# Optimization experiments

Hardware: AMD Instinct MI355X
Metric: run time of the kernel (lower is better)

The kernel has to match this reference:

```python
import jax, jax.numpy as jnp
import numpy as np

B, H, D, S = 8, 12, 64, 1024


def setup_inputs() -> dict:
    key = jax.random.key(0)
    kq, kk, kv, km = jax.random.split(key, 4)
    Q = jax.random.normal(kq, (B, H, D, S), dtype=jnp.float32)
    K = jax.random.normal(kk, (B, H, D, S), dtype=jnp.float32)
    V = jax.random.normal(kv, (B, H, D, S), dtype=jnp.float32)
    atten_masks = jax.random.randint(km, (B, S), 0, 2, dtype=jnp.int32)
    return {"Q": Q, "K": K, "V": V, "atten_masks": atten_masks}


def reference(Q, K, V, atten_masks):
    # Q,K,V: [B, H, D, S] (feature-major layout as in the torch module)
    d_k = Q.shape[2]
    # scores = K^T @ Q / sqrt(d_k) -> [B, H, S_k, S_q]
    scores = jnp.einsum('bhds,bhdt->bhst', K, Q) / jnp.sqrt(jnp.float32(d_k))
    # mask [B, S] applies along the LAST axis (query index) after the cat-broadcast
    mask = atten_masks[:, None, None, :]  # [B,1,1,S] broadcasts to [B,H,S,S]
    scores = jnp.where(mask == 0, jnp.float32(-1e9), scores)
    # softmax over last dim (faithful to dim=-1 in the original)
    attn = jax.nn.softmax(scores, axis=-1)  # [B, H, S_k, S_q]
    # context = V @ attn -> [B, H, D, S_q]
    context = jnp.einsum('bhds,bhst->bhdt', V, attn)
    # transpose(-1,-2) -> [B, H, S, D]; concat heads along feature dim -> [B, S, H*D]
    context = jnp.transpose(context, (0, 3, 1, 2)).reshape(context.shape[0], context.shape[3], -1)
    return (context, attn)
```

## Files before the change

kernel.cpp:

```cpp
#include <hip/hip_runtime.h>
#include <stdint.h>


typedef __attribute__((ext_vector_type(8))) short short8;
typedef __attribute__((ext_vector_type(4))) float floatx4;

#define DEVINL __device__ __forceinline__

DEVINL uint32_t f2u(float x) { union { float f; uint32_t u; } c; c.f = x; return c.u; }
DEVINL float u2f(uint32_t u) { union { uint32_t u; float f; } c; c.u = u; return c.f; }

DEVINL void split_bf16(float x, short &hi, short &lo) {
  uint32_t u = f2u(x);
  uint32_t r = u + 0x7FFFu + ((u >> 16) & 1u);
  hi = (short)(r >> 16);
  float hf = u2f(r & 0xFFFF0000u);
  float lf = x - hf;
  uint32_t v = f2u(lf);
  uint32_t r2 = v + 0x7FFFu + ((v >> 16) & 1u);
  lo = (short)(r2 >> 16);
}

__global__ void k0_qtranspose(const float* __restrict__ Q, unsigned short* __restrict__ QT) {
  const int bh = blockIdx.y;
  const int t0 = blockIdx.x * 64;
  const int tid = threadIdx.x;
  __shared__ float tile[64][65];
  {
    const int d = tid >> 2;
    const int ts = (tid & 3) * 16;
    const float* src = Q + ((size_t)bh * 64 + d) * 1024 + t0 + ts;
    #pragma unroll
    for (int i = 0; i < 4; ++i) {
      float4 v = reinterpret_cast<const float4*>(src)[i];
      tile[d][ts + 4 * i + 0] = v.x;
      tile[d][ts + 4 * i + 1] = v.y;
      tile[d][ts + 4 * i + 2] = v.z;
      tile[d][ts + 4 * i + 3] = v.w;
    }
  }
  __syncthreads();
  {
    const int t = tid >> 2;
    const int dseg = (tid & 3) * 16;
    uint32_t hw[8], lw[8];
    #pragma unroll
    for (int jj = 0; jj < 8; ++jj) {
      short h0, l0, h1, l1;
      split_bf16(tile[dseg + 2 * jj + 0][t], h0, l0);
      split_bf16(tile[dseg + 2 * jj + 1][t], h1, l1);
      hw[jj] = (uint32_t)(uint16_t)h0 | ((uint32_t)(uint16_t)h1 << 16);
      lw[jj] = (uint32_t)(uint16_t)l0 | ((uint32_t)(uint16_t)l1 << 16);
    }
    unsigned short* orow = QT + ((size_t)bh * 1024 + t0 + t) * 128;
    uint4* oh = reinterpret_cast<uint4*>(orow + dseg);
    oh[0] = make_uint4(hw[0], hw[1], hw[2], hw[3]);
    oh[1] = make_uint4(hw[4], hw[5], hw[6], hw[7]);
    uint4* ol = reinterpret_cast<uint4*>(orow + 64 + dseg);
    ol[0] = make_uint4(lw[0], lw[1], lw[2], lw[3]);
    ol[1] = make_uint4(lw[4], lw[5], lw[6], lw[7]);
  }
}

__global__ __launch_bounds__(256, 2)
void k1_scores_softmax(const float* __restrict__ Kt, const int* __restrict__ masks,
                       const unsigned short* __restrict__ QT, float* __restrict__ attn) {
  const int bh = blockIdx.y;
  const int b = bh / 12;
  const int sblk = blockIdx.x;
  const int tid = threadIdx.x;
  const int wave = tid >> 6, lane = tid & 63;
  const int ws = wave >> 1, wt = wave & 1;
  const int q = lane >> 4, l15 = lane & 15;

  short8 ahi[2], alo[2];
  {
    const int sA = sblk * 32 + ws * 16 + l15;
    const float* Kp = Kt + (size_t)bh * 65536 + sA;
    #pragma unroll
    for (int kk = 0; kk < 2; ++kk)
      #pragma unroll
      for (int j = 0; j < 8; ++j) {
        short h, l;
        split_bf16(Kp[(size_t)(kk * 32 + q * 8 + j) * 1024], h, l);
        ahi[kk][j] = h; alo[kk][j] = l;
      }
  }

  floatx4 acc[8][4];
  #pragma unroll
  for (int i = 0; i < 8; ++i)
    #pragma unroll
    for (int j = 0; j < 4; ++j) acc[i][j] = (floatx4){0.f, 0.f, 0.f, 0.f};

  const unsigned short* QTb = QT + (size_t)bh * 1024 * 128;
  #pragma unroll
  for (int tt = 0; tt < 8; ++tt) {
    #pragma unroll
    for (int nf = 0; nf < 4; ++nf) {
      const int t = tt * 128 + wt * 64 + nf * 16 + l15;
      const unsigned short* row = QTb + (size_t)t * 128 + q * 8;
      #pragma unroll
      for (int kk = 0; kk < 2; ++kk) {
        short8 bh16 = *reinterpret_cast<const short8*>(row + kk * 32);
        short8 bl16 = *reinterpret_cast<const short8*>(row + 64 + kk * 32);
        acc[tt][nf] = __builtin_amdgcn_mfma_f32_16x16x32_bf16(ahi[kk], bh16, acc[tt][nf], 0, 0, 0);
        acc[tt][nf] = __builtin_amdgcn_mfma_f32_16x16x32_bf16(alo[kk], bh16, acc[tt][nf], 0, 0, 0);
        acc[tt][nf] = __builtin_amdgcn_mfma_f32_16x16x32_bf16(ahi[kk], bl16, acc[tt][nf], 0, 0, 0);
      }
    }
  }

  const int* mrow = masks + b * 1024;
  float mx[4] = {-3.0e38f, -3.0e38f, -3.0e38f, -3.0e38f};
  #pragma unroll
  for (int tt = 0; tt < 8; ++tt)
    #pragma unroll
    for (int nf = 0; nf < 4; ++nf) {
      const int t = tt * 128 + wt * 64 + nf * 16 + l15;
      const bool mk = (mrow[t] != 0);
      #pragma unroll
      for (int r = 0; r < 4; ++r) {
        float v = mk ? acc[tt][nf][r] * 0.125f : -1.0e9f;
        acc[tt][nf][r] = v;
        mx[r] = fmaxf(mx[r], v);
      }
    }
  #pragma unroll
  for (int r = 0; r < 4; ++r)
    #pragma unroll
    for (int off = 1; off < 16; off <<= 1)
      mx[r] = fmaxf(mx[r], __shfl_xor(mx[r], off, 16));

  __shared__ float redmax[2][32];
  __shared__ float redsum[2][32];
  const int srow = ws * 16 + q * 4;
  if (l15 == 0) {
    #pragma unroll
    for (int r = 0; r < 4; ++r) redmax[wt][srow + r] = mx[r];
  }
  __syncthreads();
  float fm[4];
  #pragma unroll
  for (int r = 0; r < 4; ++r) fm[r] = fmaxf(redmax[0][srow + r], redmax[1][srow + r]);

  float sm[4] = {0.f, 0.f, 0.f, 0.f};
  #pragma unroll
  for (int tt = 0; tt < 8; ++tt)
    #pragma unroll
    for (int nf = 0; nf < 4; ++nf)
      #pragma unroll
      for (int r = 0; r < 4; ++r) {
        float e = __expf(acc[tt][nf][r] - fm[r]);
        acc[tt][nf][r] = e;
        sm[r] += e;
      }
  #pragma unroll
  for (int r = 0; r < 4; ++r)
    #pragma unroll
    for (int off = 1; off < 16; off <<= 1)
      sm[r] += __shfl_xor(sm[r], off, 16);
  if (l15 == 0) {
    #pragma unroll
    for (int r = 0; r < 4; ++r) redsum[wt][srow + r] = sm[r];
  }
  __syncthreads();
  float inv[4];
  #pragma unroll
  for (int r = 0; r < 4; ++r) inv[r] = 1.0f / (redsum[0][srow + r] + redsum[1][srow + r]);

  float* arow = attn + (size_t)bh * 1024 * 1024;
  #pragma unroll
  for (int tt = 0; tt < 8; ++tt)
    #pragma unroll
    for (int nf = 0; nf < 4; ++nf) {
      const int t = tt * 128 + wt * 64 + nf * 16 + l15;
      #pragma unroll
      for (int r = 0; r < 4; ++r) {
        const int s = sblk * 32 + srow + r;
        arow[(size_t)s * 1024 + t] = acc[tt][nf][r] * inv[r];
      }
    }
}

__global__ __launch_bounds__(256, 2)
void k2_pv(const float* __restrict__ V, const float* __restrict__ attn, float* __restrict__ ctx) {
  const int bh = blockIdx.y;
  const int b = bh / 12, h = bh % 12;
  const int tblk = blockIdx.x;
  const int tid = threadIdx.x;
  const int wave = tid >> 6, lane = tid & 63;
  const int q = lane >> 4, l15 = lane & 15;
  const int twave = tblk * 128 + wave * 32;

  floatx4 acc[4][2];
  #pragma unroll
  for (int i = 0; i < 4; ++i)
    #pragma unroll
    for (int j = 0; j < 2; ++j) acc[i][j] = (floatx4){0.f, 0.f, 0.f, 0.f};

  const float* Vb = V + (size_t)bh * 65536;
  const float* Ab = attn + (size_t)bh * 1048576;

  for (int s0 = 0; s0 < 1024; s0 += 32) {
    short8 vhi[4], vlo[4];
    #pragma unroll
    for (int mf = 0; mf < 4; ++mf) {
      const float* p = Vb + (size_t)(mf * 16 + l15) * 1024 + s0 + q * 8;
      #pragma unroll
      for (int j = 0; j < 8; ++j) {
        short hh, ll; split_bf16(p[j], hh, ll);
        vhi[mf][j] = hh; vlo[mf][j] = ll;
      }
    }
    short8 phi[2], plo[2];
    #pragma unroll
    for (int nf = 0; nf < 2; ++nf) {
      const int t = twave + nf * 16 + l15;
      const float* ap = Ab + (size_t)(s0 + q * 8) * 1024 + t;
      #pragma unroll
      for (int j = 0; j < 8; ++j) {
        short hh, ll; split_bf16(ap[(size_t)j * 1024], hh, ll);
        phi[nf][j] = hh; plo[nf][j] = ll;
      }
    }
    #pragma unroll
    for (int mf = 0; mf < 4; ++mf)
      #pragma unroll
      for (int nf = 0; nf < 2; ++nf) {
        acc[mf][nf] = __builtin_amdgcn_mfma_f32_16x16x32_bf16(vhi[mf], phi[nf], acc[mf][nf], 0, 0, 0);
        acc[mf][nf] = __builtin_amdgcn_mfma_f32_16x16x32_bf16(vlo[mf], phi[nf], acc[mf][nf], 0, 0, 0);
        acc[mf][nf] = __builtin_amdgcn_mfma_f32_16x16x32_bf16(vhi[mf], plo[nf], acc[mf][nf], 0, 0, 0);
      }
  }
  #pragma unroll
  for (int mf = 0; mf < 4; ++mf)
    #pragma unroll
    for (int nf = 0; nf < 2; ++nf) {
      const int t = twave + nf * 16 + l15;
      const int d0 = mf * 16 + q * 4;
      float* op = ctx + ((size_t)b * 1024 + t) * 768 + h * 64 + d0;
      *reinterpret_cast<floatx4*>(op) = acc[mf][nf];
    }
}

extern "C" void kernel_launch(void* const* d_in, const int* in_sizes, int n_in,
                              void* d_out, int out_size, void* d_ws, size_t ws_size,
                              hipStream_t stream) {
  const float* Q = (const float*)d_in[0];
  const float* K = (const float*)d_in[1];
  const float* V = (const float*)d_in[2];
  const int* masks = (const int*)d_in[3];
  float* ctx = (float*)d_out;
  float* attn = (float*)d_out + (size_t)8 * 1024 * 768;
  unsigned short* QT = (unsigned short*)d_ws;

  k0_qtranspose<<<dim3(16, 96), 256, 0, stream>>>(Q, QT);
  k1_scores_softmax<<<dim3(32, 96), 256, 0, stream>>>(K, masks, QT, attn);
  k2_pv<<<dim3(8, 96), 256, 0, stream>>>(V, attn, ctx);
}
```

Measured before the change: 835.9 us.

## Drop split-bf16 in PV, skip softmax max pass, retile scores kernel

```diff
diff --git a/kernel.cpp b/kernel.cpp
--- a/kernel.cpp
+++ b/kernel.cpp
@@ -9,6 +9,12 @@
 
 DEVINL uint32_t f2u(float x) { union { float f; uint32_t u; } c; c.f = x; return c.u; }
 DEVINL float u2f(uint32_t u) { union { uint32_t u; float f; } c; c.u = u; return c.f; }
+
+DEVINL short cvt_bf16(float x) {
+  uint32_t u = f2u(x);
+  uint32_t r = u + 0x7FFFu + ((u >> 16) & 1u);
+  return (short)(r >> 16);
+}
 
 DEVINL void split_bf16(float x, short &hi, short &lo) {
   uint32_t u = f2u(x);
@@ -62,21 +68,19 @@
   }
 }
 
-__global__ __launch_bounds__(256, 2)
+__global__ __launch_bounds__(256, 4)
 void k1_scores_softmax(const float* __restrict__ Kt, const int* __restrict__ masks,
                        const unsigned short* __restrict__ QT, float* __restrict__ attn) {
-  const int bh = blockIdx.y;
+  const int bh = blockIdx.x;
   const int b = bh / 12;
-  const int sblk = blockIdx.x;
+  const int s0 = blockIdx.y * 16;
   const int tid = threadIdx.x;
-  const int wave = tid >> 6, lane = tid & 63;
-  const int ws = wave >> 1, wt = wave & 1;
+  const int w = tid >> 6, lane = tid & 63;
   const int q = lane >> 4, l15 = lane & 15;
 
   short8 ahi[2], alo[2];
   {
-    const int sA = sblk * 32 + ws * 16 + l15;
-    const float* Kp = Kt + (size_t)bh * 65536 + sA;
+    const float* Kp = Kt + (size_t)bh * 65536 + s0 + l15;
     #pragma unroll
     for (int kk = 0; kk < 2; ++kk)
       #pragma unroll
@@ -87,107 +91,75 @@
       }
   }
 
-  floatx4 acc[8][4];
-  #pragma unroll
-  for (int i = 0; i < 8; ++i)
-    #pragma unroll
-    for (int j = 0; j < 4; ++j) acc[i][j] = (floatx4){0.f, 0.f, 0.f, 0.f};
-
-  const unsigned short* QTb = QT + (size_t)bh * 1024 * 128;
-  #pragma unroll
-  for (int tt = 0; tt < 8; ++tt) {
-    #pragma unroll
-    for (int nf = 0; nf < 4; ++nf) {
-      const int t = tt * 128 + wt * 64 + nf * 16 + l15;
-      const unsigned short* row = QTb + (size_t)t * 128 + q * 8;
-      #pragma unroll
-      for (int kk = 0; kk < 2; ++kk) {
-        short8 bh16 = *reinterpret_cast<const short8*>(row + kk * 32);
-        short8 bl16 = *reinterpret_cast<const short8*>(row + 64 + kk * 32);
-        acc[tt][nf] = __builtin_amdgcn_mfma_f32_16x16x32_bf16(ahi[kk], bh16, acc[tt][nf], 0, 0, 0);
-        acc[tt][nf] = __builtin_amdgcn_mfma_f32_16x16x32_bf16(alo[kk], bh16, acc[tt][nf], 0, 0, 0);
-        acc[tt][nf] = __builtin_amdgcn_mfma_f32_16x16x32_bf16(ahi[kk], bl16, acc[tt][nf], 0, 0, 0);
-      }
-    }
-  }
-
   const int* mrow = masks + b * 1024;
-  float mx[4] = {-3.0e38f, -3.0e38f, -3.0e38f, -3.0e38f};
-  #pragma unroll
-  for (int tt = 0; tt < 8; ++tt)
-    #pragma unroll
-    for (int nf = 0; nf < 4; ++nf) {
-      const int t = tt * 128 + wt * 64 + nf * 16 + l15;
-      const bool mk = (mrow[t] != 0);
-      #pragma unroll
-      for (int r = 0; r < 4; ++r) {
-        float v = mk ? acc[tt][nf][r] * 0.125f : -1.0e9f;
-        acc[tt][nf][r] = v;
-        mx[r] = fmaxf(mx[r], v);
-      }
-    }
-  #pragma unroll
-  for (int r = 0; r < 4; ++r)
-    #pragma unroll
-    for (int off = 1; off < 16; off <<= 1)
-      mx[r] = fmaxf(mx[r], __shfl_xor(mx[r], off, 16));
-
-  __shared__ float redmax[2][32];
-  __shared__ float redsum[2][32];
-  const int srow = ws * 16 + q * 4;
-  if (l15 == 0) {
-    #pragma unroll
-    for (int r = 0; r < 4; ++r) redmax[wt][srow + r] = mx[r];
-  }
-  __syncthreads();
-  float fm[4];
-  #pragma unroll
-  for (int r = 0; r < 4; ++r) fm[r] = fmaxf(redmax[0][srow + r], redmax[1][srow + r]);
+  uint32_t mkbits = 0;
+  #pragma unroll
+  for (int nf = 0; nf < 16; ++nf)
+    mkbits |= (mrow[w * 256 + nf * 16 + l15] != 0 ? 1u : 0u) << nf;
+
+  floatx4 acc[16];
+  #pragma unroll
+  for (int i = 0; i < 16; ++i) acc[i] = (floatx4){0.f, 0.f, 0.f, 0.f};
+
+  const unsigned short* QTb = QT + (size_t)bh * 131072;
+  #pragma unroll
+  for (int nf = 0; nf < 16; ++nf) {
+    const int t = w * 256 + nf * 16 + l15;
+    const unsigned short* row = QTb + (size_t)t * 128 + q * 8;
+    #pragma unroll
+    for (int kk = 0; kk < 2; ++kk) {
+      short8 bhh = *reinterpret_cast<const short8*>(row + kk * 32);
+      short8 bll = *reinterpret_cast<const short8*>(row + 64 + kk * 32);
+      acc[nf] = __builtin_amdgcn_mfma_f32_16x16x32_bf16(ahi[kk], bhh, acc[nf], 0, 0, 0);
+      acc[nf] = __builtin_amdgcn_mfma_f32_16x16x32_bf16(alo[kk], bhh, acc[nf], 0, 0, 0);
+      acc[nf] = __builtin_amdgcn_mfma_f32_16x16x32_bf16(ahi[kk], bll, acc[nf], 0, 0, 0);
+    }
+  }
 
   float sm[4] = {0.f, 0.f, 0.f, 0.f};
   #pragma unroll
-  for (int tt = 0; tt < 8; ++tt)
-    #pragma unroll
-    for (int nf = 0; nf < 4; ++nf)
-      #pragma unroll
-      for (int r = 0; r < 4; ++r) {
-        float e = __expf(acc[tt][nf][r] - fm[r]);
-        acc[tt][nf][r] = e;
-        sm[r] += e;
-      }
+  for (int nf = 0; nf < 16; ++nf) {
+    const bool mk = (mkbits >> nf) & 1u;
+    #pragma unroll
+    for (int r = 0; r < 4; ++r) {
+      float e = mk ? __expf(acc[nf][r] * 0.125f) : 0.0f;
+      acc[nf][r] = e;
+      sm[r] += e;
+    }
+  }
   #pragma unroll
   for (int r = 0; r < 4; ++r)
     #pragma unroll
     for (int off = 1; off < 16; off <<= 1)
       sm[r] += __shfl_xor(sm[r], off, 16);
+
+  __shared__ float redsum[4][16];
   if (l15 == 0) {
     #pragma unroll
-    for (int r = 0; r < 4; ++r) redsum[wt][srow + r] = sm[r];
+    for (int r = 0; r < 4; ++r) redsum[w][q * 4 + r] = sm[r];
   }
   __syncthreads();
   float inv[4];
   #pragma unroll
-  for (int r = 0; r < 4; ++r) inv[r] = 1.0f / (redsum[0][srow + r] + redsum[1][srow + r]);
-
-  float* arow = attn + (size_t)bh * 1024 * 1024;
-  #pragma unroll
-  for (int tt = 0; tt < 8; ++tt)
-    #pragma unroll
-    for (int nf = 0; nf < 4; ++nf) {
-      const int t = tt * 128 + wt * 64 + nf * 16 + l15;
-      #pragma unroll
-      for (int r = 0; r < 4; ++r) {
-        const int s = sblk * 32 + srow + r;
-        arow[(size_t)s * 1024 + t] = acc[tt][nf][r] * inv[r];
-      }
-    }
-}
-
-__global__ __launch_bounds__(256, 2)
+  for (int r = 0; r < 4; ++r)
+    inv[r] = 1.0f / (redsum[0][q * 4 + r] + redsum[1][q * 4 + r] +
+                     redsum[2][q * 4 + r] + redsum[3][q * 4 + r]);
+
+  float* arow = attn + (size_t)bh * 1048576 + (size_t)s0 * 1024;
+  #pragma unroll
+  for (int nf = 0; nf < 16; ++nf) {
+    const int t = w * 256 + nf * 16 + l15;
+    #pragma unroll
+    for (int r = 0; r < 4; ++r)
+      arow[(size_t)(q * 4 + r) * 1024 + t] = acc[nf][r] * inv[r];
+  }
+}
+
+__global__ __launch_bounds__(256, 4)
 void k2_pv(const float* __restrict__ V, const float* __restrict__ attn, float* __restrict__ ctx) {
-  const int bh = blockIdx.y;
+  const int bh = blockIdx.x;
   const int b = bh / 12, h = bh % 12;
-  const int tblk = blockIdx.x;
+  const int tblk = blockIdx.y;
   const int tid = threadIdx.x;
   const int wave = tid >> 6, lane = tid & 63;
   const int q = lane >> 4, l15 = lane & 15;
@@ -203,35 +175,30 @@
   const float* Ab = attn + (size_t)bh * 1048576;
 
   for (int s0 = 0; s0 < 1024; s0 += 32) {
-    short8 vhi[4], vlo[4];
+    short8 va[4];
     #pragma unroll
     for (int mf = 0; mf < 4; ++mf) {
       const float* p = Vb + (size_t)(mf * 16 + l15) * 1024 + s0 + q * 8;
-      #pragma unroll
-      for (int j = 0; j < 8; ++j) {
-        short hh, ll; split_bf16(p[j], hh, ll);
-        vhi[mf][j] = hh; vlo[mf][j] = ll;
-      }
-    }
-    short8 phi[2], plo[2];
+      float4 v0 = *reinterpret_cast<const float4*>(p);
+      float4 v1 = *reinterpret_cast<const float4*>(p + 4);
+      va[mf][0] = cvt_bf16(v0.x); va[mf][1] = cvt_bf16(v0.y);
+      va[mf][2] = cvt_bf16(v0.z); va[mf][3] = cvt_bf16(v0.w);
+      va[mf][4] = cvt_bf16(v1.x); va[mf][5] = cvt_bf16(v1.y);
+      va[mf][6] = cvt_bf16(v1.z); va[mf][7] = cvt_bf16(v1.w);
+    }
+    short8 pa[2];
     #pragma unroll
     for (int nf = 0; nf < 2; ++nf) {
       const int t = twave + nf * 16 + l15;
       const float* ap = Ab + (size_t)(s0 + q * 8) * 1024 + t;
       #pragma unroll
-      for (int j = 0; j < 8; ++j) {
-        short hh, ll; split_bf16(ap[(size_t)j * 1024], hh, ll);
-        phi[nf][j] = hh; plo[nf][j] = ll;
-      }
+      for (int j = 0; j < 8; ++j) pa[nf][j] = cvt_bf16(ap[(size_t)j * 1024]);
     }
     #pragma unroll
     for (int mf = 0; mf < 4; ++mf)
       #pragma unroll
-      for (int nf = 0; nf < 2; ++nf) {
-        acc[mf][nf] = __builtin_amdgcn_mfma_f32_16x16x32_bf16(vhi[mf], phi[nf], acc[mf][nf], 0, 0, 0);
-        acc[mf][nf] = __builtin_amdgcn_mfma_f32_16x16x32_bf16(vlo[mf], phi[nf], acc[mf][nf], 0, 0, 0);
-        acc[mf][nf] = __builtin_amdgcn_mfma_f32_16x16x32_bf16(vhi[mf], plo[nf], acc[mf][nf], 0, 0, 0);
-      }
+      for (int nf = 0; nf < 2; ++nf)
+        acc[mf][nf] = __builtin_amdgcn_mfma_f32_16x16x32_bf16(va[mf], pa[nf], acc[mf][nf], 0, 0, 0);
   }
   #pragma unroll
   for (int mf = 0; mf < 4; ++mf)
@@ -256,6 +223,6 @@
   unsigned short* QT = (unsigned short*)d_ws;
 
   k0_qtranspose<<<dim3(16, 96), 256, 0, stream>>>(Q, QT);
-  k1_scores_softmax<<<dim3(32, 96), 256, 0, stream>>>(K, masks, QT, attn);
-  k2_pv<<<dim3(8, 96), 256, 0, stream>>>(V, attn, ctx);
-}
+  k1_scores_softmax<<<dim3(96, 64), 256, 0, stream>>>(K, masks, QT, attn);
+  k2_pv<<<dim3(96, 8), 256, 0, stream>>>(V, attn, ctx);
+}
```

Measured after the change: 803.7 us. 1.04x faster.
